# Kernel tuning notes

Measured on AMD Instinct MI355X. Metric: run time of the kernel, lower is better.

Reference implementation:

```python
import jax, jax.numpy as jnp
import numpy as np

BS, C, H, W = 8, 64, 256, 256
N_MODE_1, N_MODE_2 = 32, 32  # retained modes along H-rfft and W-rfft


def setup_inputs() -> dict:
    key = jax.random.key(0)
    ks = jax.random.split(key, 5)
    ci = co = C // 2
    scale = 1.0 / (C * C)  # module's self.scale flavor; kaiming init approximated by scaled normal
    return {
        "x": jax.random.normal(ks[0], (BS, C, H, W), jnp.float32),
        "w1_re": jax.random.normal(ks[1], (2, ci, co, N_MODE_1), jnp.float32) * 0.05,
        "w1_im": jax.random.normal(ks[2], (2, ci, co, N_MODE_1), jnp.float32) * 0.05,
        "w2_re": jax.random.normal(ks[3], (2, ci, co, N_MODE_2), jnp.float32) * 0.05,
        "w2_im": jax.random.normal(ks[4], (2, ci, co, N_MODE_2), jnp.float32) * 0.05,
    }


def reference(x, w1_re, w1_im, w2_re, w2_im):
    bs, c, h, w = x.shape
    x5 = x.reshape(bs, 2, c // 2, h, w)  # split channels into 2 groups

    # ---- spectral conv along W (dim=-1), weight_2 ----
    w2c = w2_re + 1j * w2_im  # [2, ci, co, n_mode_2]
    x_ft = jnp.fft.rfft(x5, axis=-1, norm="ortho")  # [bs,2,ci,h,w//2+1]
    out_ft = jnp.einsum("bgixy,gioy->bgoxy", x_ft[..., :N_MODE_2], w2c)
    out_ft = jnp.pad(out_ft, ((0, 0), (0, 0), (0, 0), (0, 0), (0, x_ft.shape[-1] - N_MODE_2)))
    x5 = jnp.fft.irfft(out_ft, n=w, axis=-1, norm="ortho")

    # ---- spectral conv along H (dim=-2), weight_1 ----
    w1c = w1_re + 1j * w1_im  # [2, ci, co, n_mode_1]
    x_ft = jnp.fft.rfft(x5, axis=-2, norm="ortho")  # [bs,2,ci,h//2+1,w]
    out_ft = jnp.einsum("bgixy,giox->bgoxy", x_ft[..., :N_MODE_1, :], w1c)
    out_ft = jnp.pad(out_ft, ((0, 0), (0, 0), (0, 0), (0, x_ft.shape[-2] - N_MODE_1), (0, 0)))
    x5 = jnp.fft.irfft(out_ft, n=h, axis=-2, norm="ortho")

    return x5.reshape(bs, c, h, w)
```

## Files before the change

kernel.cpp:

```cpp
#include <hip/hip_runtime.h>
#include <math.h>

#define PI2_256 0.0245436926061702596754894014318f

__global__ __launch_bounds__(256) void init_tab(float* __restrict__ tc, float* __restrict__ ts) {
    int idx = blockIdx.x * 256 + threadIdx.x;
    int k = idx >> 8, n = idx & 255;
    int m = (k * n) & 255;
    float s, c;
    sincosf(PI2_256 * (float)m, &s, &c);
    tc[idx] = c;
    ts[idx] = s;
}

__global__ __launch_bounds__(256) void w_fwd(const float* __restrict__ x,
                                             const float* __restrict__ w2r,
                                             const float* __restrict__ w2i,
                                             float* __restrict__ Yw) {
    __shared__ float tile[32 * 256];
    __shared__ float XrL[32 * 36], XiL[32 * 36];

    const int bid  = blockIdx.x;
    const int xrow = bid & 255;
    const int g    = (bid >> 8) & 1;
    const int b    = bid >> 9;
    const int t    = threadIdx.x;

    const size_t chan0 = (size_t)(b * 64 + g * 32);
    const size_t base  = (chan0 * 256 + xrow) * 256;

    {
        const int wq = t & 63, i0 = t >> 6;
        #pragma unroll
        for (int r = 0; r < 8; ++r) {
            const int i = i0 + r * 4;
            *(float4*)(tile + i * 256 + wq * 4) =
                *(const float4*)(x + base + (size_t)i * 65536 + wq * 4);
        }
    }
    __syncthreads();

    {
        const int hq = t & 31, i0 = t >> 5;
        const int h0 = hq * 4;
        float4 a4[4]; float m0[4], m1[4], m2[4], m3[4]; float x128v[4];
        #pragma unroll
        for (int r = 0; r < 4; ++r) {
            const float* row = tile + (i0 + r * 8) * 256;
            a4[r] = *(const float4*)(row + h0);
            m0[r] = row[(256 - (h0 + 0)) & 255];
            m1[r] = row[256 - (h0 + 1)];
            m2[r] = row[256 - (h0 + 2)];
            m3[r] = row[256 - (h0 + 3)];
            x128v[r] = row[128];
        }
        __syncthreads();
        #pragma unroll
        for (int r = 0; r < 4; ++r) {
            float* row = tile + (i0 + r * 8) * 256;
            float4 ye = make_float4(a4[r].x + m0[r], a4[r].y + m1[r],
                                    a4[r].z + m2[r], a4[r].w + m3[r]);
            float4 yo = make_float4(a4[r].x - m0[r], a4[r].y - m1[r],
                                    a4[r].z - m2[r], a4[r].w - m3[r]);
            if (hq == 0) yo.x = x128v[r];
            *(float4*)(row + h0)       = ye;
            *(float4*)(row + 128 + h0) = yo;
        }
    }
    __syncthreads();

    {
        const int k = t & 31, i4 = t >> 5;
        float sd, cd; sincosf(PI2_256 * (float)k, &sd, &cd);
        const float t2 = 2.f * cd;
        float cA = 1.f, sA = 0.f;
        float cB = cd,  sB = -sd;
        const float* r0 = tile + i4 * 256;
        const float* r1 = r0 + 8 * 256;
        const float* r2 = r0 + 16 * 256;
        const float* r3 = r0 + 24 * 256;
        const float x0_0 = r0[0] * 0.5f, x128_0 = r0[128];
        const float x0_1 = r1[0] * 0.5f, x128_1 = r1[128];
        const float x0_2 = r2[0] * 0.5f, x128_2 = r2[128];
        const float x0_3 = r3[0] * 0.5f, x128_3 = r3[128];
        const float sgn = (k & 1) ? -1.f : 1.f;
        float xr0 = sgn * x128_0 - x0_0, xi0 = 0.f;
        float xr1 = sgn * x128_1 - x0_1, xi1 = 0.f;
        float xr2 = sgn * x128_2 - x0_2, xi2 = 0.f;
        float xr3 = sgn * x128_3 - x0_3, xi3 = 0.f;
        for (int hq = 0; hq < 32; ++hq) {
            const float4 yeA = *(const float4*)(r0 + hq * 4);
            const float4 yoA = *(const float4*)(r0 + 128 + hq * 4);
            const float4 yeB = *(const float4*)(r1 + hq * 4);
            const float4 yoB = *(const float4*)(r1 + 128 + hq * 4);
            const float4 yeC = *(const float4*)(r2 + hq * 4);
            const float4 yoC = *(const float4*)(r2 + 128 + hq * 4);
            const float4 yeD = *(const float4*)(r3 + hq * 4);
            const float4 yoD = *(const float4*)(r3 + 128 + hq * 4);
            #pragma unroll
            for (int j = 0; j < 4; ++j) {
                const float c = cA, s = sA;
                xr0 += (&yeA.x)[j] * c;  xi0 -= (&yoA.x)[j] * s;
                xr1 += (&yeB.x)[j] * c;  xi1 -= (&yoB.x)[j] * s;
                xr2 += (&yeC.x)[j] * c;  xi2 -= (&yoC.x)[j] * s;
                xr3 += (&yeD.x)[j] * c;  xi3 -= (&yoD.x)[j] * s;
                const float cn = t2 * cA - cB; cB = cA; cA = cn;
                const float sn = t2 * sA - sB; sB = sA; sA = sn;
            }
        }
        XrL[(i4     ) * 36 + k] = xr0;  XiL[(i4     ) * 36 + k] = xi0;
        XrL[(i4 +  8) * 36 + k] = xr1;  XiL[(i4 +  8) * 36 + k] = xi1;
        XrL[(i4 + 16) * 36 + k] = xr2;  XiL[(i4 + 16) * 36 + k] = xi2;
        XrL[(i4 + 24) * 36 + k] = xr3;  XiL[(i4 + 24) * 36 + k] = xi3;
    }
    __syncthreads();

    {
        const int kq = t & 7, o = t >> 3;
        const int k4 = kq * 4;
        float4 ar = {0,0,0,0}, ai = {0,0,0,0};
        const float* wrb = w2r + (size_t)g * 32768 + o * 32 + k4;
        const float* wib = w2i + (size_t)g * 32768 + o * 32 + k4;
        for (int i = 0; i < 32; ++i) {
            const float4 xr = *(const float4*)(XrL + i * 36 + k4);
            const float4 xi = *(const float4*)(XiL + i * 36 + k4);
            const float4 wr = *(const float4*)(wrb + i * 1024);
            const float4 wi = *(const float4*)(wib + i * 1024);
            ar.x += xr.x * wr.x - xi.x * wi.x;  ai.x += xr.x * wi.x + xi.x * wr.x;
            ar.y += xr.y * wr.y - xi.y * wi.y;  ai.y += xr.y * wi.y + xi.y * wr.y;
            ar.z += xr.z * wr.z - xi.z * wi.z;  ai.z += xr.z * wi.z + xi.z * wr.z;
            ar.w += xr.w * wr.w - xi.w * wi.w;  ai.w += xr.w * wi.w + xi.w * wr.w;
        }
        const float s2 = 2.f / 256.f, s1 = 1.f / 256.f;
        const float s0 = (k4 == 0) ? s1 : s2;
        float* dst = Yw + (size_t)((b * 2 + g) * 32 + o) * 16384 + (size_t)xrow * 64 + k4;
        *(float4*)(dst)      = make_float4(ar.x * s0, ar.y * s2, ar.z * s2, ar.w * s2);
        *(float4*)(dst + 32) = make_float4(ai.x * s0, ai.y * s2, ai.z * s2, ai.w * s2);
    }
}

__global__ __launch_bounds__(256) void h_fwd(const float* __restrict__ Yw,
                                             const float* __restrict__ tc,
                                             const float* __restrict__ ts,
                                             float* __restrict__ Z) {
    __shared__ float YL[256 * 64];
    const int bid = blockIdx.x;
    const int t = threadIdx.x;
    {
        const float* src = Yw + (size_t)bid * 16384;
        #pragma unroll
        for (int r = 0; r < 16; ++r) {
            const int f = t + r * 256;
            *(float4*)(YL + f * 4) = *(const float4*)(src + f * 4);
        }
    }
    __syncthreads();

    const int s = t & 63, khg = t >> 6;
    const float y0 = YL[s], y128 = YL[128 * 64 + s];
    float xr[8], xi[8];
    #pragma unroll
    for (int r = 0; r < 8; ++r) {
        xr[r] = ((r & 1) ? -y128 : y128) - y0;
        xi[r] = 0.f;
    }
    const int kb = khg * 8;
    for (int hq = 0; hq < 32; ++hq) {
        float ye[4], yo[4];
        #pragma unroll
        for (int j = 0; j < 4; ++j) {
            const int h = hq * 4 + j;
            const float a = YL[h * 64 + s];
            const float m = YL[((256 - h) & 255) * 64 + s];
            ye[j] = a + m;  yo[j] = a - m;
        }
        #pragma unroll
        for (int r = 0; r < 8; ++r) {
            const float4 c4 = *(const float4*)(tc + (size_t)(kb + r) * 256 + hq * 4);
            const float4 s4 = *(const float4*)(ts + (size_t)(kb + r) * 256 + hq * 4);
            xr[r] += ye[0] * c4.x + ye[1] * c4.y + ye[2] * c4.z + ye[3] * c4.w;
            xi[r] -= yo[0] * s4.x + yo[1] * s4.y + yo[2] * s4.z + yo[3] * s4.w;
        }
    }
    const int o = bid & 31, bg = bid >> 5;
    #pragma unroll
    for (int r = 0; r < 8; ++r) {
        const size_t zi_ = (((size_t)bg * 32 + (kb + r)) * 32 + o) * 128 + s;
        Z[zi_]      = xr[r];
        Z[zi_ + 64] = xi[r];
    }
}

__global__ __launch_bounds__(256) void h_mix2(const float* __restrict__ Z,
                                              const float* __restrict__ w1r,
                                              const float* __restrict__ w1i,
                                              float* __restrict__ Z2) {
    __shared__ float ZL[32 * 128];
    __shared__ float WrL[1024], WiL[1024];
    const int bid = blockIdx.x;
    const int kh = bid & 31, bg = bid >> 5;
    const int g = bg & 1;
    const int t = threadIdx.x;
    {
        const float* src = Z + (size_t)bid * 4096;
        #pragma unroll
        for (int r = 0; r < 4; ++r) {
            const int f = t + r * 256;
            *(float4*)(ZL + f * 4) = *(const float4*)(src + f * 4);
        }
        #pragma unroll
        for (int r = 0; r < 4; ++r) {
            const int idx = t + r * 256;
            const int gidx = g * 32768 + (idx >> 5) * 1024 + (idx & 31) * 32 + kh;
            WrL[idx] = w1r[gidx];
            WiL[idx] = w1i[gidx];
        }
    }
    __syncthreads();

    const int s = t & 63, og = t >> 6;
    float accr[8], acci[8];
    #pragma unroll
    for (int m = 0; m < 8; ++m) { accr[m] = 0.f; acci[m] = 0.f; }
    for (int i = 0; i < 32; ++i) {
        const float zr = ZL[i * 128 + s];
        const float zi = ZL[i * 128 + 64 + s];
        #pragma unroll
        for (int m = 0; m < 8; ++m) {
            const int o = og * 8 + m;
            const float wr = WrL[i * 32 + o];
            const float wi = WiL[i * 32 + o];
            accr[m] += zr * wr - zi * wi;
            acci[m] += zr * wi + zi * wr;
        }
    }
    const float sck = (kh == 0) ? (1.f / 256.f) : (2.f / 256.f);
    #pragma unroll
    for (int m = 0; m < 8; ++m) {
        const int o = og * 8 + m;
        const size_t zo = ((size_t)(bg * 32 + o) * 32 + kh) * 128 + s;
        Z2[zo]      = accr[m] * sck;
        Z2[zo + 64] = acci[m] * sck;
    }
}

__global__ __launch_bounds__(256) void h_inv2(const float* __restrict__ Z2,
                                              const float* __restrict__ tc,
                                              const float* __restrict__ ts,
                                              float* __restrict__ YHg) {
    __shared__ float ZL[32 * 128];
    __shared__ float TcL[32 * 128], TsL[32 * 128];
    const int bid = blockIdx.x;
    const int t = threadIdx.x;
    {
        const float* src = Z2 + (size_t)bid * 4096;
        #pragma unroll
        for (int r = 0; r < 4; ++r) {
            const int f = t + r * 256;
            *(float4*)(ZL + f * 4) = *(const float4*)(src + f * 4);
        }
        #pragma unroll
        for (int r = 0; r < 4; ++r) {
            const int q = t + r * 256;
            const int k = q >> 5, hq = q & 31;
            *(float4*)(TcL + k * 128 + hq * 4) = *(const float4*)(tc + (size_t)k * 256 + hq * 4);
            *(float4*)(TsL + k * 128 + hq * 4) = *(const float4*)(ts + (size_t)k * 256 + hq * 4);
        }
    }
    __syncthreads();

    const int s = t & 63, hg = t >> 6;
    float zr[32], zi[32];
    #pragma unroll
    for (int k = 0; k < 32; ++k) {
        zr[k] = ZL[k * 128 + s];
        zi[k] = ZL[k * 128 + 64 + s];
    }
    float* dst = YHg + (size_t)bid * 16384;
    #pragma unroll
    for (int jq = 0; jq < 8; ++jq) {
        const int h0 = hg * 32 + jq * 4;
        float sC[4] = {0, 0, 0, 0}, sS[4] = {0, 0, 0, 0};
        #pragma unroll
        for (int k = 0; k < 32; ++k) {
            const float4 c4 = *(const float4*)(TcL + k * 128 + h0);
            const float4 s4 = *(const float4*)(TsL + k * 128 + h0);
            sC[0] += zr[k] * c4.x;  sS[0] += zi[k] * s4.x;
            sC[1] += zr[k] * c4.y;  sS[1] += zi[k] * s4.y;
            sC[2] += zr[k] * c4.z;  sS[2] += zi[k] * s4.z;
            sC[3] += zr[k] * c4.w;  sS[3] += zi[k] * s4.w;
        }
        #pragma unroll
        for (int jj = 0; jj < 4; ++jj) {
            const int h = h0 + jj;
            dst[h * 64 + s] = sC[jj] - sS[jj];
            if (h > 0) dst[(256 - h) * 64 + s] = sC[jj] + sS[jj];
        }
    }
    if (hg == 0) {
        float ny = 0.f;
        #pragma unroll
        for (int k = 0; k < 32; ++k) ny += (k & 1) ? -zr[k] : zr[k];
        dst[128 * 64 + s] = ny;
    }
}

__global__ __launch_bounds__(256) void w_inv2(const float* __restrict__ YHg,
                                              const float* __restrict__ tc,
                                              const float* __restrict__ ts,
                                              float* __restrict__ out) {
    __shared__ float YL[32 * 64];
    __shared__ float TcL[32 * 128], TsL[32 * 128];
    const int bid = blockIdx.x;
    const int hb = bid & 7, c = bid >> 3;
    const int t = threadIdx.x;
    {
        const float* src = YHg + (size_t)c * 16384 + hb * 2048;
        #pragma unroll
        for (int r = 0; r < 2; ++r) {
            const int f = t + r * 256;
            *(float4*)(YL + f * 4) = *(const float4*)(src + f * 4);
        }
        #pragma unroll
        for (int r = 0; r < 4; ++r) {
            const int q = t + r * 256;
            const int k = q >> 5, wq_ = q & 31;
            *(float4*)(TcL + k * 128 + wq_ * 4) = *(const float4*)(tc + (size_t)k * 256 + wq_ * 4);
            *(float4*)(TsL + k * 128 + wq_ * 4) = *(const float4*)(ts + (size_t)k * 256 + wq_ * 4);
        }
    }
    __syncthreads();

    const int wq = t & 31, hh = t >> 5;
    const int w0 = wq * 4;
    float* outp = out + (size_t)c * 65536;

    float sC[4][4], sS[4][4];
    #pragma unroll
    for (int j = 0; j < 4; ++j)
        #pragma unroll
        for (int jj = 0; jj < 4; ++jj) { sC[j][jj] = 0.f; sS[j][jj] = 0.f; }

    for (int k = 0; k < 32; ++k) {
        const float4 c4 = *(const float4*)(TcL + k * 128 + w0);
        const float4 s4 = *(const float4*)(TsL + k * 128 + w0);
        #pragma unroll
        for (int j = 0; j < 4; ++j) {
            const int hl = hh * 4 + j;
            const float R = YL[hl * 64 + k];
            const float I = YL[hl * 64 + 32 + k];
            sC[j][0] += R * c4.x;  sS[j][0] += I * s4.x;
            sC[j][1] += R * c4.y;  sS[j][1] += I * s4.y;
            sC[j][2] += R * c4.z;  sS[j][2] += I * s4.z;
            sC[j][3] += R * c4.w;  sS[j][3] += I * s4.w;
        }
    }
    #pragma unroll
    for (int j = 0; j < 4; ++j) {
        const int h = hb * 32 + hh * 4 + j;
        *(float4*)(outp + (size_t)h * 256 + w0) =
            make_float4(sC[j][0] - sS[j][0], sC[j][1] - sS[j][1],
                        sC[j][2] - sS[j][2], sC[j][3] - sS[j][3]);
        #pragma unroll
        for (int jj = 0; jj < 4; ++jj) {
            const int w = w0 + jj;
            if (w >= 1) outp[(size_t)h * 256 + 256 - w] = sC[j][jj] + sS[j][jj];
        }
    }
    if (wq == 0) {
        #pragma unroll
        for (int j = 0; j < 4; ++j) {
            const int hl = hh * 4 + j;
            const int h = hb * 32 + hl;
            float ny = 0.f;
            #pragma unroll
            for (int k = 0; k < 32; ++k) {
                const float R = YL[hl * 64 + k];
                ny += (k & 1) ? -R : R;
            }
            outp[(size_t)h * 256 + 128] = ny;
        }
    }
}

extern "C" void kernel_launch(void* const* d_in, const int* in_sizes, int n_in,
                              void* d_out, int out_size, void* d_ws, size_t ws_size,
                              hipStream_t stream) {
    const float* x   = (const float*)d_in[0];
    const float* w1r = (const float*)d_in[1];
    const float* w1i = (const float*)d_in[2];
    const float* w2r = (const float*)d_in[3];
    const float* w2i = (const float*)d_in[4];
    float* out = (float*)d_out;
    float* ws  = (float*)d_ws;

    float* tc = ws;
    float* ts = ws + 8192;
    float* Yw = ws + 16384;
    float* Z  = Yw + 8388608;
    float* Z2 = Z + 2097152;

    init_tab<<<32, 256, 0, stream>>>(tc, ts);
    w_fwd<<<4096, 256, 0, stream>>>(x, w2r, w2i, Yw);
    h_fwd<<<512, 256, 0, stream>>>(Yw, tc, ts, Z);
    h_mix2<<<512, 256, 0, stream>>>(Z, w1r, w1i, Z2);
    h_inv2<<<512, 256, 0, stream>>>(Z2, tc, ts, Yw);
    w_inv2<<<4096, 256, 0, stream>>>(Yw, tc, ts, out);
}
```

Baseline: 216.9 us.

## Split DFT sums across thread pairs and pad shared tile in forward kernels

The w_fwd DFT stage is re-tiled so each thread computes four frequencies over two rows and half the input, combining halves with a lane shuffle. The shared tile gets a padded row stride to reduce bank conflicts. h_fwd replaces global twiddle-table loads with per-thread Chebyshev recurrences, uses float4 LDS reads over four columns and splits the sum across lane pairs. This cuts shared and global memory traffic per FMA, at the cost of more registers and extra sincos setup.

```diff
diff --git a/kernel.cpp b/kernel.cpp
--- a/kernel.cpp
+++ b/kernel.cpp
@@ -2,6 +2,7 @@
 #include <math.h>
 
 #define PI2_256 0.0245436926061702596754894014318f
+#define TS 260
 
 __global__ __launch_bounds__(256) void init_tab(float* __restrict__ tc, float* __restrict__ ts) {
     int idx = blockIdx.x * 256 + threadIdx.x;
@@ -17,7 +18,7 @@
                                              const float* __restrict__ w2r,
                                              const float* __restrict__ w2i,
                                              float* __restrict__ Yw) {
-    __shared__ float tile[32 * 256];
+    __shared__ float tile[32 * TS];
     __shared__ float XrL[32 * 36], XiL[32 * 36];
 
     const int bid  = blockIdx.x;
@@ -34,7 +35,7 @@
         #pragma unroll
         for (int r = 0; r < 8; ++r) {
             const int i = i0 + r * 4;
-            *(float4*)(tile + i * 256 + wq * 4) =
+            *(float4*)(tile + i * TS + wq * 4) =
                 *(const float4*)(x + base + (size_t)i * 65536 + wq * 4);
         }
     }
@@ -46,7 +47,7 @@
         float4 a4[4]; float m0[4], m1[4], m2[4], m3[4]; float x128v[4];
         #pragma unroll
         for (int r = 0; r < 4; ++r) {
-            const float* row = tile + (i0 + r * 8) * 256;
+            const float* row = tile + (i0 + r * 8) * TS;
             a4[r] = *(const float4*)(row + h0);
             m0[r] = row[(256 - (h0 + 0)) & 255];
             m1[r] = row[256 - (h0 + 1)];
@@ -57,7 +58,7 @@
         __syncthreads();
         #pragma unroll
         for (int r = 0; r < 4; ++r) {
-            float* row = tile + (i0 + r * 8) * 256;
+            float* row = tile + (i0 + r * 8) * TS;
             float4 ye = make_float4(a4[r].x + m0[r], a4[r].y + m1[r],
                                     a4[r].z + m2[r], a4[r].w + m3[r]);
             float4 yo = make_float4(a4[r].x - m0[r], a4[r].y - m1[r],
@@ -70,48 +71,70 @@
     __syncthreads();
 
     {
-        const int k = t & 31, i4 = t >> 5;
-        float sd, cd; sincosf(PI2_256 * (float)k, &sd, &cd);
-        const float t2 = 2.f * cd;
-        float cA = 1.f, sA = 0.f;
-        float cB = cd,  sB = -sd;
-        const float* r0 = tile + i4 * 256;
-        const float* r1 = r0 + 8 * 256;
-        const float* r2 = r0 + 16 * 256;
-        const float* r3 = r0 + 24 * 256;
-        const float x0_0 = r0[0] * 0.5f, x128_0 = r0[128];
-        const float x0_1 = r1[0] * 0.5f, x128_1 = r1[128];
-        const float x0_2 = r2[0] * 0.5f, x128_2 = r2[128];
-        const float x0_3 = r3[0] * 0.5f, x128_3 = r3[128];
-        const float sgn = (k & 1) ? -1.f : 1.f;
-        float xr0 = sgn * x128_0 - x0_0, xi0 = 0.f;
-        float xr1 = sgn * x128_1 - x0_1, xi1 = 0.f;
-        float xr2 = sgn * x128_2 - x0_2, xi2 = 0.f;
-        float xr3 = sgn * x128_3 - x0_3, xi3 = 0.f;
-        for (int hq = 0; hq < 32; ++hq) {
-            const float4 yeA = *(const float4*)(r0 + hq * 4);
-            const float4 yoA = *(const float4*)(r0 + 128 + hq * 4);
-            const float4 yeB = *(const float4*)(r1 + hq * 4);
-            const float4 yoB = *(const float4*)(r1 + 128 + hq * 4);
-            const float4 yeC = *(const float4*)(r2 + hq * 4);
-            const float4 yoC = *(const float4*)(r2 + 128 + hq * 4);
-            const float4 yeD = *(const float4*)(r3 + hq * 4);
-            const float4 yoD = *(const float4*)(r3 + 128 + hq * 4);
+        const int hs = t & 1;
+        const int kg = (t >> 1) & 7;
+        const int rg = t >> 4;
+        const float* rp0 = tile + (2 * rg) * TS;
+        const float* rp1 = rp0 + TS;
+        const float sgn = (kg & 1) ? -1.f : 1.f;
+        const int hb = hs * 64;
+
+        float cA[4], sA[4], cB[4], sB[4], t2[4];
+        float xr[4][2], xi[4][2];
+        #pragma unroll
+        for (int kk = 0; kk < 4; ++kk) {
+            const int k = kg + 8 * kk;
+            float sd, cd; sincosf(PI2_256 * (float)k, &sd, &cd);
+            t2[kk] = 2.f * cd;
+            float ss, cc;
+            sincosf(PI2_256 * (float)((k * hb) & 255), &ss, &cc);
+            cA[kk] = cc; sA[kk] = ss;
+            sincosf(PI2_256 * (float)((k * (hb - 1)) & 255), &ss, &cc);
+            cB[kk] = cc; sB[kk] = ss;
+        }
+        const float x0_0 = rp0[0] * 0.5f, x128_0 = rp0[128];
+        const float x0_1 = rp1[0] * 0.5f, x128_1 = rp1[128];
+        #pragma unroll
+        for (int kk = 0; kk < 4; ++kk) {
+            xr[kk][0] = (hs == 0) ? (sgn * x128_0 - x0_0) : 0.f;
+            xr[kk][1] = (hs == 0) ? (sgn * x128_1 - x0_1) : 0.f;
+            xi[kk][0] = 0.f; xi[kk][1] = 0.f;
+        }
+        for (int hq = 0; hq < 16; ++hq) {
+            const float4 ye0 = *(const float4*)(rp0 + hb + hq * 4);
+            const float4 yo0 = *(const float4*)(rp0 + 128 + hb + hq * 4);
+            const float4 ye1 = *(const float4*)(rp1 + hb + hq * 4);
+            const float4 yo1 = *(const float4*)(rp1 + 128 + hb + hq * 4);
             #pragma unroll
             for (int j = 0; j < 4; ++j) {
-                const float c = cA, s = sA;
-                xr0 += (&yeA.x)[j] * c;  xi0 -= (&yoA.x)[j] * s;
-                xr1 += (&yeB.x)[j] * c;  xi1 -= (&yoB.x)[j] * s;
-                xr2 += (&yeC.x)[j] * c;  xi2 -= (&yoC.x)[j] * s;
-                xr3 += (&yeD.x)[j] * c;  xi3 -= (&yoD.x)[j] * s;
-                const float cn = t2 * cA - cB; cB = cA; cA = cn;
-                const float sn = t2 * sA - sB; sB = sA; sA = sn;
+                const float e0 = (&ye0.x)[j], o0 = (&yo0.x)[j];
+                const float e1 = (&ye1.x)[j], o1 = (&yo1.x)[j];
+                #pragma unroll
+                for (int kk = 0; kk < 4; ++kk) {
+                    xr[kk][0] += e0 * cA[kk];  xi[kk][0] -= o0 * sA[kk];
+                    xr[kk][1] += e1 * cA[kk];  xi[kk][1] -= o1 * sA[kk];
+                    const float cn = t2[kk] * cA[kk] - cB[kk]; cB[kk] = cA[kk]; cA[kk] = cn;
+                    const float sn = t2[kk] * sA[kk] - sB[kk]; sB[kk] = sA[kk]; sA[kk] = sn;
+                }
             }
         }
-        XrL[(i4     ) * 36 + k] = xr0;  XiL[(i4     ) * 36 + k] = xi0;
-        XrL[(i4 +  8) * 36 + k] = xr1;  XiL[(i4 +  8) * 36 + k] = xi1;
-        XrL[(i4 + 16) * 36 + k] = xr2;  XiL[(i4 + 16) * 36 + k] = xi2;
-        XrL[(i4 + 24) * 36 + k] = xr3;  XiL[(i4 + 24) * 36 + k] = xi3;
+        #pragma unroll
+        for (int kk = 0; kk < 4; ++kk)
+            #pragma unroll
+            for (int r = 0; r < 2; ++r) {
+                xr[kk][r] += __shfl_xor(xr[kk][r], 1);
+                xi[kk][r] += __shfl_xor(xi[kk][r], 1);
+            }
+        if (hs == 0) {
+            #pragma unroll
+            for (int kk = 0; kk < 4; ++kk) {
+                const int k = kg + 8 * kk;
+                XrL[(2 * rg    ) * 36 + k] = xr[kk][0];
+                XiL[(2 * rg    ) * 36 + k] = xi[kk][0];
+                XrL[(2 * rg + 1) * 36 + k] = xr[kk][1];
+                XiL[(2 * rg + 1) * 36 + k] = xi[kk][1];
+            }
+        }
     }
     __syncthreads();
 
@@ -140,8 +163,6 @@
 }
 
 __global__ __launch_bounds__(256) void h_fwd(const float* __restrict__ Yw,
-                                             const float* __restrict__ tc,
-                                             const float* __restrict__ ts,
                                              float* __restrict__ Z) {
     __shared__ float YL[256 * 64];
     const int bid = blockIdx.x;
@@ -156,38 +177,66 @@
     }
     __syncthreads();
 
-    const int s = t & 63, khg = t >> 6;
-    const float y0 = YL[s], y128 = YL[128 * 64 + s];
-    float xr[8], xi[8];
-    #pragma unroll
-    for (int r = 0; r < 8; ++r) {
-        xr[r] = ((r & 1) ? -y128 : y128) - y0;
-        xi[r] = 0.f;
-    }
-    const int kb = khg * 8;
-    for (int hq = 0; hq < 32; ++hq) {
+    const int hs = t & 1, kg = (t >> 1) & 7, sp = t >> 4;
+    const int hb = hs * 64;
+    const float sgn = (kg & 1) ? -1.f : 1.f;
+    const float4 y0q   = *(const float4*)(YL + sp * 4);
+    const float4 y128q = *(const float4*)(YL + 128 * 64 + sp * 4);
+
+    float cA[4], sA[4], cB[4], sB[4], t2[4];
+    float xr[4][4], xi[4][4];
+    #pragma unroll
+    for (int kk = 0; kk < 4; ++kk) {
+        const int k = kg + 8 * kk;
+        float sd, cd; sincosf(PI2_256 * (float)k, &sd, &cd);
+        t2[kk] = 2.f * cd;
+        float ss, cc;
+        sincosf(PI2_256 * (float)((k * hb) & 255), &ss, &cc);
+        cA[kk] = cc; sA[kk] = ss;
+        sincosf(PI2_256 * (float)((k * (hb - 1)) & 255), &ss, &cc);
+        cB[kk] = cc; sB[kk] = ss;
+        #pragma unroll
+        for (int j = 0; j < 4; ++j) {
+            xr[kk][j] = (hs == 0) ? (sgn * (&y128q.x)[j] - (&y0q.x)[j]) : 0.f;
+            xi[kk][j] = 0.f;
+        }
+    }
+    for (int h = hb; h < hb + 64; ++h) {
+        const float4 aq = *(const float4*)(YL + h * 64 + sp * 4);
+        const float4 mq = *(const float4*)(YL + ((256 - h) & 255) * 64 + sp * 4);
         float ye[4], yo[4];
         #pragma unroll
         for (int j = 0; j < 4; ++j) {
-            const int h = hq * 4 + j;
-            const float a = YL[h * 64 + s];
-            const float m = YL[((256 - h) & 255) * 64 + s];
-            ye[j] = a + m;  yo[j] = a - m;
-        }
-        #pragma unroll
-        for (int r = 0; r < 8; ++r) {
-            const float4 c4 = *(const float4*)(tc + (size_t)(kb + r) * 256 + hq * 4);
-            const float4 s4 = *(const float4*)(ts + (size_t)(kb + r) * 256 + hq * 4);
-            xr[r] += ye[0] * c4.x + ye[1] * c4.y + ye[2] * c4.z + ye[3] * c4.w;
-            xi[r] -= yo[0] * s4.x + yo[1] * s4.y + yo[2] * s4.z + yo[3] * s4.w;
-        }
-    }
-    const int o = bid & 31, bg = bid >> 5;
-    #pragma unroll
-    for (int r = 0; r < 8; ++r) {
-        const size_t zi_ = (((size_t)bg * 32 + (kb + r)) * 32 + o) * 128 + s;
-        Z[zi_]      = xr[r];
-        Z[zi_ + 64] = xi[r];
+            ye[j] = (&aq.x)[j] + (&mq.x)[j];
+            yo[j] = (&aq.x)[j] - (&mq.x)[j];
+        }
+        #pragma unroll
+        for (int kk = 0; kk < 4; ++kk) {
+            #pragma unroll
+            for (int j = 0; j < 4; ++j) {
+                xr[kk][j] += ye[j] * cA[kk];
+                xi[kk][j] -= yo[j] * sA[kk];
+            }
+            const float cn = t2[kk] * cA[kk] - cB[kk]; cB[kk] = cA[kk]; cA[kk] = cn;
+            const float sn = t2[kk] * sA[kk] - sB[kk]; sB[kk] = sA[kk]; sA[kk] = sn;
+        }
+    }
+    #pragma unroll
+    for (int kk = 0; kk < 4; ++kk)
+        #pragma unroll
+        for (int j = 0; j < 4; ++j) {
+            xr[kk][j] += __shfl_xor(xr[kk][j], 1);
+            xi[kk][j] += __shfl_xor(xi[kk][j], 1);
+        }
+    if (hs == 0) {
+        const int o = bid & 31, bg = bid >> 5;
+        #pragma unroll
+        for (int kk = 0; kk < 4; ++kk) {
+            const int k = kg + 8 * kk;
+            const size_t zi_ = (((size_t)bg * 32 + k) * 32 + o) * 128 + sp * 4;
+            *(float4*)(Z + zi_)      = make_float4(xr[kk][0], xr[kk][1], xr[kk][2], xr[kk][3]);
+            *(float4*)(Z + zi_ + 64) = make_float4(xi[kk][0], xi[kk][1], xi[kk][2], xi[kk][3]);
+        }
     }
 }
 
@@ -402,7 +451,7 @@
 
     init_tab<<<32, 256, 0, stream>>>(tc, ts);
     w_fwd<<<4096, 256, 0, stream>>>(x, w2r, w2i, Yw);
-    h_fwd<<<512, 256, 0, stream>>>(Yw, tc, ts, Z);
+    h_fwd<<<512, 256, 0, stream>>>(Yw, Z);
     h_mix2<<<512, 256, 0, stream>>>(Z, w1r, w1i, Z2);
     h_inv2<<<512, 256, 0, stream>>>(Z2, tc, ts, Yw);
     w_inv2<<<4096, 256, 0, stream>>>(Yw, tc, ts, out);
```

Measured after the change: 193.7 us. 10.7% less time.
